# Performance work log

Hardware: AMD Instinct MI355X
Metric: run time of the kernel (lower is better)

The kernel has to match this reference:

```python
import jax, jax.numpy as jnp
import numpy as np

N_RAYS = 65536   # 256x256 image
T_SAMPLES = 128  # StratifiedRayStepSampler default
HID = 16         # tiny radiance-field MLP hidden width


def setup_inputs() -> dict:
    key = jax.random.key(0)
    ks = jax.random.split(key, 8)
    o = jax.random.normal(ks[0], (N_RAYS, 3), jnp.float32)
    d = jax.random.normal(ks[1], (N_RAYS, 3), jnp.float32)
    tnear = jnp.zeros((N_RAYS, 1), jnp.float32)
    # tfar in [1,5): guarantees tfar > tnear for every ray
    tfar = 1.0 + 4.0 * jax.random.uniform(ks[2], (N_RAYS, 1), jnp.float32)
    noise = jax.random.uniform(ks[3], (T_SAMPLES, N_RAYS, 1), jnp.float32)
    W1 = jax.random.normal(ks[4], (3, HID), jnp.float32) * 0.5
    b1 = jnp.zeros((HID,), jnp.float32)
    w_sigma = jax.random.normal(ks[5], (HID, 1), jnp.float32) * 0.5
    W_rgb = jax.random.normal(ks[6], (HID, 3), jnp.float32) * 0.5
    return {"o": o, "d": d, "tnear": tnear, "tfar": tfar, "noise": noise,
            "W1": W1, "b1": b1, "w_sigma": w_sigma, "W_rgb": W_rgb}


def reference(o, d, tnear, tfar, noise, W1, b1, w_sigma, W_rgb):
    T = noise.shape[0]
    dnorm = jnp.linalg.norm(d, axis=-1, keepdims=True)            # (N,1)
    # stratified sampling: ts[i] = tnear + (tfar-tnear)*(i+u_i)/T  -> (T,N,1)
    bins = (jnp.arange(T, dtype=o.dtype)[:, None, None] + noise) / T
    ts = tnear[None] + (tfar - tnear)[None] * bins                # (T,N,1)
    # evaluate rays and query radiance field
    xyz = o[None] + ts * d[None]                                  # (T,N,3)
    h = jax.nn.relu(xyz @ W1 + b1)                                # (T,N,HID)
    sigma = jax.nn.softplus(h @ w_sigma)                          # (T,N,1) density
    rgb = jax.nn.sigmoid(h @ W_rgb)                               # (T,N,3) color
    # volumetric integration along sample axis
    delta = jnp.concatenate([ts[1:] - ts[:-1], tfar[None] - ts[-1:]], axis=0)
    sd = sigma * delta * dnorm[None]                              # (T,N,1)
    # exclusive cumsum -> log-transmittance (stable cumprod)
    log_trans = jnp.concatenate(
        [jnp.zeros_like(sd[:1]), -jnp.cumsum(sd[:-1], axis=0)], axis=0)
    weights = jnp.exp(log_trans) * (1.0 - jnp.exp(-sd))           # (T,N,1)
    color = jnp.sum(weights * rgb, axis=0)                        # (N,3)
    depth = jnp.sum(weights * ts, axis=0)                         # (N,1)
    alpha = jnp.sum(weights, axis=0)                              # (N,1)
    return jnp.concatenate([color, depth, alpha], axis=-1)        # (N,5)
```

## Files before the change

kernel.cpp:

```cpp
#include <hip/hip_runtime.h>
#include <math.h>

#define N_RAYS 65536
#define T_SAMPLES 128
#define HID 16

__global__ __launch_bounds__(256) void radiance_kernel(
    const float* __restrict__ o,
    const float* __restrict__ d,
    const float* __restrict__ tnear,
    const float* __restrict__ tfar,
    const float* __restrict__ noise,
    const float* __restrict__ W1,
    const float* __restrict__ b1,
    const float* __restrict__ w_sigma,
    const float* __restrict__ W_rgb,
    float* __restrict__ out)
{
    const int ray = blockIdx.x * blockDim.x + threadIdx.x;
    if (ray >= N_RAYS) return;

    const float ox = o[ray*3+0], oy = o[ray*3+1], oz = o[ray*3+2];
    const float dx = d[ray*3+0], dy = d[ray*3+1], dz = d[ray*3+2];
    const float tn = tnear[ray];
    const float tf = tfar[ray];
    const float dnorm = sqrtf(dx*dx + dy*dy + dz*dz);
    const float range = tf - tn;
    const float invT = 1.0f / (float)T_SAMPLES;

    float A[HID], B[HID];
#pragma unroll
    for (int j = 0; j < HID; ++j) {
        const float w0 = W1[0*HID + j], w1 = W1[1*HID + j], w2 = W1[2*HID + j];
        A[j] = fmaf(ox, w0, fmaf(oy, w1, fmaf(oz, w2, b1[j])));
        B[j] = fmaf(dx, w0, fmaf(dy, w1, dz * w2));
    }
    float WS[HID], WR[HID], WG[HID], WB[HID];
#pragma unroll
    for (int j = 0; j < HID; ++j) {
        WS[j] = w_sigma[j];
        WR[j] = W_rgb[j*3+0];
        WG[j] = W_rgb[j*3+1];
        WB[j] = W_rgb[j*3+2];
    }

    float trans = 1.0f;
    float cr = 0.f, cg = 0.f, cb = 0.f, cd = 0.f, ca = 0.f;
    float p_ts = 0.f, p_sig = 0.f, p_r = 0.f, p_g = 0.f, p_b = 0.f;

    float nz = noise[ray];
    for (int t = 0; t < T_SAMPLES; ++t) {
        const float ts = fmaf(range, ((float)t + nz) * invT, tn);
        if (t + 1 < T_SAMPLES) nz = noise[(size_t)(t+1)*N_RAYS + ray];

        float sp = 0.f, rr = 0.f, gg = 0.f, bb = 0.f;
#pragma unroll
        for (int j = 0; j < HID; ++j) {
            const float h = fmaxf(fmaf(ts, B[j], A[j]), 0.0f);
            sp = fmaf(h, WS[j], sp);
            rr = fmaf(h, WR[j], rr);
            gg = fmaf(h, WG[j], gg);
            bb = fmaf(h, WB[j], bb);
        }
        const float e = __expf(-fabsf(sp));
        const float sigma = fmaxf(sp, 0.0f) + __logf(1.0f + e);
        const float r = __builtin_amdgcn_rcpf(1.0f + __expf(-rr));
        const float g = __builtin_amdgcn_rcpf(1.0f + __expf(-gg));
        const float b = __builtin_amdgcn_rcpf(1.0f + __expf(-bb));

        if (t > 0) {
            const float delta = ts - p_ts;
            const float sd = p_sig * delta * dnorm;
            const float et = __expf(-sd);
            const float w = trans * (1.0f - et);
            cr = fmaf(w, p_r, cr);
            cg = fmaf(w, p_g, cg);
            cb = fmaf(w, p_b, cb);
            cd = fmaf(w, p_ts, cd);
            ca += w;
            trans *= et;
        }
        p_ts = ts; p_sig = sigma; p_r = r; p_g = g; p_b = b;
    }
    {
        const float delta = tf - p_ts;
        const float sd = p_sig * delta * dnorm;
        const float et = __expf(-sd);
        const float w = trans * (1.0f - et);
        cr = fmaf(w, p_r, cr);
        cg = fmaf(w, p_g, cg);
        cb = fmaf(w, p_b, cb);
        cd = fmaf(w, p_ts, cd);
        ca += w;
    }

    out[ray*5+0] = cr;
    out[ray*5+1] = cg;
    out[ray*5+2] = cb;
    out[ray*5+3] = cd;
    out[ray*5+4] = ca;
}

extern "C" void kernel_launch(void* const* d_in, const int* in_sizes, int n_in,
                              void* d_out, int out_size, void* d_ws, size_t ws_size,
                              hipStream_t stream) {
    const float* o       = (const float*)d_in[0];
    const float* d       = (const float*)d_in[1];
    const float* tnear   = (const float*)d_in[2];
    const float* tfar    = (const float*)d_in[3];
    const float* noise   = (const float*)d_in[4];
    const float* W1      = (const float*)d_in[5];
    const float* b1      = (const float*)d_in[6];
    const float* w_sigma = (const float*)d_in[7];
    const float* W_rgb   = (const float*)d_in[8];
    float* out = (float*)d_out;

    dim3 block(256);
    dim3 grid((N_RAYS + 255) / 256);
    hipLaunchKernelGGL(radiance_kernel, grid, block, 0, stream,
                       o, d, tnear, tfar, noise, W1, b1, w_sigma, W_rgb, out);
}
```

Measured before the change: 122.5 us.

## Split each ray's samples across four waves and combine with transmittance scan

Each block now handles 64 rays with 4 waves, and each wave integrates a contiguous quarter of the 128 samples. The partial color, depth and alpha and the chunk transmittance go to shared memory, and wave 0 combines them by scaling each chunk by the preceding transmittance product. This raises thread-level parallelism and shortens the per-thread serial chain, at the cost of redundant per-ray setup in every wave and a block barrier. Transcendentals are also rewritten with exp2/log builtins, folding softplus directly into the transmittance exponent.

New measurement: 119.9 us. 1.02x faster.

```diff
diff --git a/kernel.cpp b/kernel.cpp
--- a/kernel.cpp
+++ b/kernel.cpp
@@ -4,6 +4,12 @@
 #define N_RAYS 65536
 #define T_SAMPLES 128
 #define HID 16
+
+#define RAYS_PER_BLOCK 64
+#define CHUNKS 4
+#define CHUNK_LEN (T_SAMPLES / CHUNKS)
+
+#define L2E 1.4426950408889634f
 
 __global__ __launch_bounds__(256) void radiance_kernel(
     const float* __restrict__ o,
@@ -17,8 +23,9 @@
     const float* __restrict__ W_rgb,
     float* __restrict__ out)
 {
-    const int ray = blockIdx.x * blockDim.x + threadIdx.x;
-    if (ray >= N_RAYS) return;
+    const int lane  = threadIdx.x & 63;
+    const int chunk = threadIdx.x >> 6;
+    const int ray   = blockIdx.x * RAYS_PER_BLOCK + lane;
 
     const float ox = o[ray*3+0], oy = o[ray*3+1], oz = o[ray*3+2];
     const float dx = d[ray*3+0], dy = d[ray*3+1], dz = d[ray*3+2];
@@ -44,14 +51,22 @@
         WB[j] = W_rgb[j*3+2];
     }
 
-    float trans = 1.0f;
+    const int t0 = chunk * CHUNK_LEN;
+    float nz = noise[(size_t)t0 * N_RAYS + ray];
+    float ts = fmaf(range, ((float)t0 + nz) * invT, tn);
+
+    float lt = 1.0f;
     float cr = 0.f, cg = 0.f, cb = 0.f, cd = 0.f, ca = 0.f;
-    float p_ts = 0.f, p_sig = 0.f, p_r = 0.f, p_g = 0.f, p_b = 0.f;
 
-    float nz = noise[ray];
-    for (int t = 0; t < T_SAMPLES; ++t) {
-        const float ts = fmaf(range, ((float)t + nz) * invT, tn);
-        if (t + 1 < T_SAMPLES) nz = noise[(size_t)(t+1)*N_RAYS + ray];
+    for (int i = 0; i < CHUNK_LEN; ++i) {
+        const int t = t0 + i;
+        float ts_next;
+        if (t + 1 < T_SAMPLES) {
+            const float nz2 = noise[(size_t)(t+1) * N_RAYS + ray];
+            ts_next = fmaf(range, ((float)(t+1) + nz2) * invT, tn);
+        } else {
+            ts_next = tf;
+        }
 
         float sp = 0.f, rr = 0.f, gg = 0.f, bb = 0.f;
 #pragma unroll
@@ -62,43 +77,54 @@
             gg = fmaf(h, WG[j], gg);
             bb = fmaf(h, WB[j], bb);
         }
-        const float e = __expf(-fabsf(sp));
-        const float sigma = fmaxf(sp, 0.0f) + __logf(1.0f + e);
-        const float r = __builtin_amdgcn_rcpf(1.0f + __expf(-rr));
-        const float g = __builtin_amdgcn_rcpf(1.0f + __expf(-gg));
-        const float b = __builtin_amdgcn_rcpf(1.0f + __expf(-bb));
 
-        if (t > 0) {
-            const float delta = ts - p_ts;
-            const float sd = p_sig * delta * dnorm;
-            const float et = __expf(-sd);
-            const float w = trans * (1.0f - et);
-            cr = fmaf(w, p_r, cr);
-            cg = fmaf(w, p_g, cg);
-            cb = fmaf(w, p_b, cb);
-            cd = fmaf(w, p_ts, cd);
-            ca += w;
-            trans *= et;
-        }
-        p_ts = ts; p_sig = sigma; p_r = r; p_g = g; p_b = b;
-    }
-    {
-        const float delta = tf - p_ts;
-        const float sd = p_sig * delta * dnorm;
-        const float et = __expf(-sd);
-        const float w = trans * (1.0f - et);
-        cr = fmaf(w, p_r, cr);
-        cg = fmaf(w, p_g, cg);
-        cb = fmaf(w, p_b, cb);
-        cd = fmaf(w, p_ts, cd);
+        const float e  = __builtin_amdgcn_exp2f(-fabsf(sp) * L2E);
+        const float l2 = fmaf(fmaxf(sp, 0.0f), L2E, __builtin_amdgcn_logf(1.0f + e));
+        const float dd = (ts_next - ts) * dnorm;
+        const float et = __builtin_amdgcn_exp2f(-dd * l2);
+
+        const float r = __builtin_amdgcn_rcpf(1.0f + __builtin_amdgcn_exp2f(-rr * L2E));
+        const float g = __builtin_amdgcn_rcpf(1.0f + __builtin_amdgcn_exp2f(-gg * L2E));
+        const float b = __builtin_amdgcn_rcpf(1.0f + __builtin_amdgcn_exp2f(-bb * L2E));
+
+        const float w = lt * (1.0f - et);
+        cr = fmaf(w, r, cr);
+        cg = fmaf(w, g, cg);
+        cb = fmaf(w, b, cb);
+        cd = fmaf(w, ts, cd);
         ca += w;
+        lt *= et;
+        ts = ts_next;
     }
 
-    out[ray*5+0] = cr;
-    out[ray*5+1] = cg;
-    out[ray*5+2] = cb;
-    out[ray*5+3] = cd;
-    out[ray*5+4] = ca;
+    __shared__ float s_lt[CHUNKS][RAYS_PER_BLOCK];
+    __shared__ float s_acc[CHUNKS][5][RAYS_PER_BLOCK];
+    s_lt[chunk][lane] = lt;
+    s_acc[chunk][0][lane] = cr;
+    s_acc[chunk][1][lane] = cg;
+    s_acc[chunk][2][lane] = cb;
+    s_acc[chunk][3][lane] = cd;
+    s_acc[chunk][4][lane] = ca;
+    __syncthreads();
+
+    if (chunk == 0) {
+        float scale = 1.0f;
+        float a0 = 0.f, a1 = 0.f, a2 = 0.f, a3 = 0.f, a4 = 0.f;
+#pragma unroll
+        for (int c = 0; c < CHUNKS; ++c) {
+            a0 = fmaf(scale, s_acc[c][0][lane], a0);
+            a1 = fmaf(scale, s_acc[c][1][lane], a1);
+            a2 = fmaf(scale, s_acc[c][2][lane], a2);
+            a3 = fmaf(scale, s_acc[c][3][lane], a3);
+            a4 = fmaf(scale, s_acc[c][4][lane], a4);
+            scale *= s_lt[c][lane];
+        }
+        out[ray*5+0] = a0;
+        out[ray*5+1] = a1;
+        out[ray*5+2] = a2;
+        out[ray*5+3] = a3;
+        out[ray*5+4] = a4;
+    }
 }
 
 extern "C" void kernel_launch(void* const* d_in, const int* in_sizes, int n_in,
@@ -115,8 +141,8 @@
     const float* W_rgb   = (const float*)d_in[8];
     float* out = (float*)d_out;
 
-    dim3 block(256);
-    dim3 grid((N_RAYS + 255) / 256);
+    dim3 block(64 * CHUNKS);
+    dim3 grid(N_RAYS / RAYS_PER_BLOCK);
     hipLaunchKernelGGL(radiance_kernel, grid, block, 0, stream,
                        o, d, tnear, tfar, noise, W1, b1, w_sigma, W_rgb, out);
 }
```
